# Performance work log

Measured on AMD Instinct MI355X. Metric: run time of the kernel, lower is better.

The kernel has to match this reference:

```python
import jax, jax.numpy as jnp
import numpy as np

N_NODES = 100000
N_EDGES = 3200000
IN_CH = 128
HID = 64
OUT_CH = 2
BN_EPS = 1e-5


def setup_inputs() -> dict:
    key = jax.random.key(0)
    ks = jax.random.split(key, 16)
    def glorot(k, shape):
        fan_in, fan_out = shape[0], shape[1]
        lim = jnp.sqrt(6.0 / (fan_in + fan_out))
        return jax.random.uniform(k, shape, jnp.float32, -lim, lim)
    inp = {
        "x": jax.random.normal(ks[0], (N_NODES, IN_CH), jnp.float32),
        "edge_index": jax.random.randint(ks[1], (2, N_EDGES), 0, N_NODES, jnp.int64),
        # input projection + input BN
        "Wp": glorot(ks[2], (IN_CH, HID)),
        "bp": jnp.zeros((HID,), jnp.float32),
        "g_in": jnp.ones((HID,), jnp.float32),
        "b_in": jnp.zeros((HID,), jnp.float32),
        # SAGEConv layer 0: lin_l (aggr, with bias) + lin_r (self, no bias)
        "Wl0": glorot(ks[3], (HID, HID)),
        "bl0": jnp.zeros((HID,), jnp.float32),
        "Wr0": glorot(ks[4], (HID, HID)),
        "g0": jnp.ones((HID,), jnp.float32),
        "b0": jnp.zeros((HID,), jnp.float32),
        # SAGEConv layer 1
        "Wl1": glorot(ks[5], (HID, HID)),
        "bl1": jnp.zeros((HID,), jnp.float32),
        "Wr1": glorot(ks[6], (HID, HID)),
        "g1": jnp.ones((HID,), jnp.float32),
        "b1": jnp.zeros((HID,), jnp.float32),
        # output head
        "Wo": glorot(ks[7], (HID, OUT_CH)),
        "bo": jnp.zeros((OUT_CH,), jnp.float32),
    }
    return inp


def _bn(h, g, b):
    # training-mode batchnorm over node dim (biased variance, as torch)
    m = h.mean(axis=0)
    v = h.var(axis=0)
    return g * (h - m) * jax.lax.rsqrt(v + BN_EPS) + b


def _sage_conv(h, src, dst, Wl, bl, Wr):
    # mean aggregation of source features at destination nodes
    msg = h[src]                                              # [E, HID]
    summed = jax.ops.segment_sum(msg, dst, num_segments=N_NODES)
    cnt = jax.ops.segment_sum(jnp.ones((src.shape[0],), h.dtype), dst,
                              num_segments=N_NODES)
    aggr = summed / jnp.maximum(cnt, 1.0)[:, None]
    return aggr @ Wl + bl + h @ Wr


def reference(x, edge_index, Wp, bp, g_in, b_in,
              Wl0, bl0, Wr0, g0, b0,
              Wl1, bl1, Wr1, g1, b1,
              Wo, bo):
    src, dst = edge_index[0], edge_index[1]
    h = jax.nn.relu(_bn(x @ Wp + bp, g_in, b_in))   # dropout: eval no-op
    h_prev = h
    # layer 0 (i=0: no residual)
    h_new = jax.nn.relu(_bn(_sage_conv(h, src, dst, Wl0, bl0, Wr0), g0, b0))
    h_prev, h = h, h_new
    # layer 1 (i=1: residual with h_prev)
    h_new = jax.nn.relu(_bn(_sage_conv(h, src, dst, Wl1, bl1, Wr1), g1, b1))
    h_new = h_new + h_prev
    h = h_new
    return h @ Wo + bo
```

## Files before the change

kernel.cpp:

```cpp
#include <hip/hip_runtime.h>
#include <hip/hip_bf16.h>

#define NN 100000
#define NE 3200000
#define IC 128
#define HD 64
#define BN_EPS 1e-5f
#define NBUK 196
#define MSB 16
#define CAP 20480

typedef __attribute__((ext_vector_type(8))) short bf16x8;
typedef __attribute__((ext_vector_type(4))) float f32x4;

#if defined(__has_builtin)
#if __has_builtin(__builtin_amdgcn_fdot2_f32_bf16)
#define HAVE_FDOT2 1
#endif
#endif
#ifndef HAVE_FDOT2
#define HAVE_FDOT2 0
#endif

#if HAVE_FDOT2
typedef __bf16 bf16x2 __attribute__((ext_vector_type(2)));
__device__ __forceinline__ float dot2acc(unsigned int pk, float acc) {
  const unsigned int one2 = 0x3F803F80u;
  return __builtin_amdgcn_fdot2_f32_bf16(__builtin_bit_cast(bf16x2, pk),
                                         __builtin_bit_cast(bf16x2, one2),
                                         acc, false);
}
#endif

__device__ __forceinline__ float bf2f(unsigned short u) {
  return __uint_as_float(((unsigned)u) << 16);
}
__device__ __forceinline__ unsigned int f2bf(float f) {
  unsigned int u = __float_as_uint(f);
  return (u + 0x7FFFu + ((u >> 16) & 1u)) >> 16;
}
__device__ __forceinline__ unsigned int pack2(float a, float b) {
  return f2bf(a) | (f2bf(b) << 16);
}

__global__ __launch_bounds__(512) void k_init(unsigned int* __restrict__ gcur,
                                              float* __restrict__ stats) {
  int t = threadIdx.x;
  if (t < 384) stats[t] = 0.f;
  if (t < NBUK) gcur[t] = (unsigned int)(t * CAP);
}

__global__ __launch_bounds__(256) void k_gemm_in(
    const float* __restrict__ x, const float* __restrict__ Wp,
    const float* __restrict__ bp, unsigned short* __restrict__ pre16,
    float* __restrict__ stats) {
  __shared__ unsigned int sXu[64 * 68];
  __shared__ uint4 sWb[16 * 64];
  __shared__ float sStS[256], sStQ[256];
  int tid = threadIdx.x;
  int wave = tid >> 6, lane = tid & 63;
  int lm = lane & 15, lb = lane >> 4;
  for (int i = tid; i < 1024; i += 256) {
    int b = i >> 6, n = i & 63;
    const float* wp = &Wp[(size_t)(8 * b) * HD + n];
    uint4 p;
    p.x = pack2(wp[0], wp[HD]);
    p.y = pack2(wp[2 * HD], wp[3 * HD]);
    p.z = pack2(wp[4 * HD], wp[5 * HD]);
    p.w = pack2(wp[6 * HD], wp[7 * HD]);
    sWb[i] = p;
  }
  float bias[4];
#pragma unroll
  for (int nt = 0; nt < 4; ++nt) bias[nt] = bp[nt * 16 + lm];
  float S[4] = {0.f, 0.f, 0.f, 0.f}, Q[4] = {0.f, 0.f, 0.f, 0.f};
  const int NT = (NN + 63) / 64;
  for (int t = blockIdx.x; t < NT; t += gridDim.x) {
    int row0 = t * 64;
    __syncthreads();
    for (int i = tid; i < 1024; i += 256) {
      int r = i >> 4, k8 = i & 15;
      int grow = row0 + r;
      uint4 p;
      if (grow < NN) {
        const float* xs = &x[(size_t)grow * IC + k8 * 8];
        float4 f0 = *(const float4*)xs;
        float4 f1 = *(const float4*)(xs + 4);
        p.x = pack2(f0.x, f0.y);
        p.y = pack2(f0.z, f0.w);
        p.z = pack2(f1.x, f1.y);
        p.w = pack2(f1.z, f1.w);
      } else {
        p.x = p.y = p.z = p.w = 0u;
      }
      *(uint4*)&sXu[r * 68 + k8 * 4] = p;
    }
    __syncthreads();
    f32x4 acc[4];
#pragma unroll
    for (int nt = 0; nt < 4; ++nt) acc[nt] = (f32x4){0.f, 0.f, 0.f, 0.f};
#pragma unroll
    for (int ks = 0; ks < 4; ++ks) {
      bf16x8 af =
          *(const bf16x8*)&sXu[(wave * 16 + lm) * 68 + ks * 16 + lb * 4];
      int b = ks * 4 + lb;
#pragma unroll
      for (int nt = 0; nt < 4; ++nt) {
        bf16x8 bf = *(const bf16x8*)&sWb[b * 64 + nt * 16 + lm];
        acc[nt] = __builtin_amdgcn_mfma_f32_16x16x32_bf16(af, bf, acc[nt],
                                                          0, 0, 0);
      }
    }
    int rowl = wave * 16 + lb * 4;
#pragma unroll
    for (int nt = 0; nt < 4; ++nt) {
#pragma unroll
      for (int r = 0; r < 4; ++r) {
        int grow = row0 + rowl + r;
        if (grow < NN) {
          float val = acc[nt][r] + bias[nt];
          pre16[(size_t)grow * HD + nt * 16 + lm] = (unsigned short)f2bf(val);
          S[nt] += val;
          Q[nt] = fmaf(val, val, Q[nt]);
        }
      }
    }
  }
#pragma unroll
  for (int nt = 0; nt < 4; ++nt) {
    S[nt] += __shfl_xor(S[nt], 16);
    S[nt] += __shfl_xor(S[nt], 32);
    Q[nt] += __shfl_xor(Q[nt], 16);
    Q[nt] += __shfl_xor(Q[nt], 32);
  }
  if (lane < 16) {
#pragma unroll
    for (int nt = 0; nt < 4; ++nt) {
      sStS[wave * 64 + nt * 16 + lane] = S[nt];
      sStQ[wave * 64 + nt * 16 + lane] = Q[nt];
    }
  }
  __syncthreads();
  if (tid < 64) {
    float Ts = sStS[tid] + sStS[64 + tid] + sStS[128 + tid] + sStS[192 + tid];
    float Tq = sStQ[tid] + sStQ[64 + tid] + sStQ[128 + tid] + sStQ[192 + tid];
    atomicAdd(&stats[tid], Ts);
    atomicAdd(&stats[64 + tid], Tq);
  }
}

__global__ __launch_bounds__(256) void k_bn_relu(
    const unsigned int* __restrict__ pre16, const float* __restrict__ stats,
    const float* __restrict__ g, const float* __restrict__ b,
    unsigned int* __restrict__ h16u) {
  size_t i = (size_t)blockIdx.x * 256 + threadIdx.x;
  int c0 = ((int)(i & 15)) * 4;
  const float invN = 1.0f / NN;
  uint2 p = *(const uint2*)&pre16[i * 2];
  float v[4];
  v[0] = __uint_as_float(p.x << 16);
  v[1] = __uint_as_float(p.x & 0xFFFF0000u);
  v[2] = __uint_as_float(p.y << 16);
  v[3] = __uint_as_float(p.y & 0xFFFF0000u);
#pragma unroll
  for (int c = 0; c < 4; ++c) {
    float m = stats[c0 + c] * invN;
    float var = stats[64 + c0 + c] * invN - m * m;
    float sc = g[c0 + c] * rsqrtf(var + BN_EPS);
    v[c] = fmaxf((v[c] - m) * sc + b[c0 + c], 0.f);
  }
  uint2 o;
  o.x = pack2(v[0], v[1]);
  o.y = pack2(v[2], v[3]);
  *(uint2*)&h16u[i * 2] = o;
}

__global__ __launch_bounds__(256) void k_msplit(
    const int* __restrict__ src, const int* __restrict__ dst,
    unsigned int* __restrict__ gcur, unsigned int* __restrict__ staging) {
  __shared__ unsigned int hist[NBUK];
  __shared__ unsigned int gbase[NBUK];
  int tid = threadIdx.x;
  for (int i = tid; i < NBUK; i += 256) hist[i] = 0u;
  __syncthreads();
  int e0 = blockIdx.x * (256 * MSB);
  unsigned int pk[MSB], rk[MSB], bk[MSB];
#pragma unroll
  for (int i = 0; i < MSB; ++i) {
    int e = e0 + i * 256 + tid;
    if (e < NE) {
      int d = dst[e];
      unsigned int b = (unsigned int)(d >> 9);
      rk[i] = atomicAdd(&hist[b], 1u);
      pk[i] = (unsigned int)src[e] | ((unsigned int)(d & 511) << 17);
      bk[i] = b;
    } else {
      bk[i] = 0xFFFFFFFFu;
    }
  }
  __syncthreads();
  for (int i = tid; i < NBUK; i += 256)
    if (hist[i]) gbase[i] = atomicAdd(&gcur[i], hist[i]);
  __syncthreads();
#pragma unroll
  for (int i = 0; i < MSB; ++i)
    if (bk[i] != 0xFFFFFFFFu) staging[gbase[bk[i]] + rk[i]] = pk[i];
}

__global__ __launch_bounds__(512) void k_bucket_sort(
    const unsigned int* __restrict__ staging,
    const unsigned int* __restrict__ gcur, unsigned int* __restrict__ nstart,
    unsigned int* __restrict__ srcoff) {
  __shared__ unsigned int hist[512];
  __shared__ unsigned int sc[512];
  __shared__ unsigned int cur[512];
  __shared__ unsigned int bs[256];
  int b = blockIdx.x, t = threadIdx.x;
  hist[t] = 0u;
  if (t < 256)
    bs[t] = (t < NBUK) ? (gcur[t] - (unsigned int)(t * CAP)) : 0u;
  __syncthreads();
  for (int off = 1; off < 256; off <<= 1) {
    unsigned int v = 0u;
    if (t < 256 && t >= off) v = bs[t - off];
    __syncthreads();
    if (t < 256) bs[t] += v;
    __syncthreads();
  }
  int lo = (b == 0) ? 0 : (int)bs[b - 1];
  int cnt = (int)bs[b] - lo;
  int base_in = b * CAP;
  for (int i = t; i < cnt; i += 512)
    atomicAdd(&hist[staging[base_in + i] >> 17], 1u);
  __syncthreads();
  unsigned int my = hist[t];
  sc[t] = my;
  __syncthreads();
  for (int off = 1; off < 512; off <<= 1) {
    unsigned int v = (t >= off) ? sc[t - off] : 0u;
    __syncthreads();
    sc[t] += v;
    __syncthreads();
  }
  unsigned int st = (unsigned int)lo + sc[t] - my;
  cur[t] = st;
  int node = b * 512 + t;
  if (node < NN) {
    nstart[node] = st;
    if (node == NN - 1) nstart[NN] = st + my;
  }
  __syncthreads();
  for (int i = t; i < cnt; i += 512) {
    unsigned int u = staging[base_in + i];
    unsigned int pos = atomicAdd(&cur[u >> 17], 1u);
    srcoff[pos] = (u & 0x1FFFFu) << 7;
  }
}

__global__ __launch_bounds__(256) void k_aggr_sorted(
    const unsigned int* __restrict__ srcoff,
    const unsigned int* __restrict__ nstart,
    const unsigned short* __restrict__ h16,
    unsigned short* __restrict__ a16) {
  int lane = threadIdx.x & 63;
  int n = (int)((blockIdx.x * 256 + threadIdx.x) >> 6);
  if (n >= NN) return;
  int g = lane >> 3;
  int q = lane & 7;
  int e0 = (int)nstart[n];
  int e1 = (int)nstart[n + 1];
  const char* hbase = (const char*)h16 + q * 16;
  float a0 = 0.f, a1 = 0.f, a2 = 0.f, a3 = 0.f;
  float a4 = 0.f, a5 = 0.f, a6 = 0.f, a7 = 0.f;
#if !HAVE_FDOT2
  float b0 = 0.f, b1 = 0.f, b2 = 0.f, b3 = 0.f;
  float b4 = 0.f, b5 = 0.f, b6 = 0.f, b7 = 0.f;
#endif
  int e = e0 + g;
  for (; e + 8 < e1; e += 16) {
    unsigned int o0 = srcoff[e];
    unsigned int o1 = srcoff[e + 8];
    uint4 u0 = *(const uint4*)(hbase + o0);
    uint4 u1 = *(const uint4*)(hbase + o1);
#if HAVE_FDOT2
    a0 = dot2acc(__builtin_amdgcn_perm(u1.x, u0.x, 0x05040100u), a0);
    a1 = dot2acc(__builtin_amdgcn_perm(u1.x, u0.x, 0x07060302u), a1);
    a2 = dot2acc(__builtin_amdgcn_perm(u1.y, u0.y, 0x05040100u), a2);
    a3 = dot2acc(__builtin_amdgcn_perm(u1.y, u0.y, 0x07060302u), a3);
    a4 = dot2acc(__builtin_amdgcn_perm(u1.z, u0.z, 0x05040100u), a4);
    a5 = dot2acc(__builtin_amdgcn_perm(u1.z, u0.z, 0x07060302u), a5);
    a6 = dot2acc(__builtin_amdgcn_perm(u1.w, u0.w, 0x05040100u), a6);
    a7 = dot2acc(__builtin_amdgcn_perm(u1.w, u0.w, 0x07060302u), a7);
#else
    a0 += __uint_as_float(u0.x << 16);
    a1 += __uint_as_float(u0.x & 0xFFFF0000u);
    a2 += __uint_as_float(u0.y << 16);
    a3 += __uint_as_float(u0.y & 0xFFFF0000u);
    a4 += __uint_as_float(u0.z << 16);
    a5 += __uint_as_float(u0.z & 0xFFFF0000u);
    a6 += __uint_as_float(u0.w << 16);
    a7 += __uint_as_float(u0.w & 0xFFFF0000u);
    b0 += __uint_as_float(u1.x << 16);
    b1 += __uint_as_float(u1.x & 0xFFFF0000u);
    b2 += __uint_as_float(u1.y << 16);
    b3 += __uint_as_float(u1.y & 0xFFFF0000u);
    b4 += __uint_as_float(u1.z << 16);
    b5 += __uint_as_float(u1.z & 0xFFFF0000u);
    b6 += __uint_as_float(u1.w << 16);
    b7 += __uint_as_float(u1.w & 0xFFFF0000u);
#endif
  }
  if (e < e1) {
    unsigned int o0 = srcoff[e];
    uint4 u0 = *(const uint4*)(hbase + o0);
#if HAVE_FDOT2
    a0 = dot2acc(__builtin_amdgcn_perm(0u, u0.x, 0x05040100u), a0);
    a1 = dot2acc(__builtin_amdgcn_perm(0u, u0.x, 0x07060302u), a1);
    a2 = dot2acc(__builtin_amdgcn_perm(0u, u0.y, 0x05040100u), a2);
    a3 = dot2acc(__builtin_amdgcn_perm(0u, u0.y, 0x07060302u), a3);
    a4 = dot2acc(__builtin_amdgcn_perm(0u, u0.z, 0x05040100u), a4);
    a5 = dot2acc(__builtin_amdgcn_perm(0u, u0.z, 0x07060302u), a5);
    a6 = dot2acc(__builtin_amdgcn_perm(0u, u0.w, 0x05040100u), a6);
    a7 = dot2acc(__builtin_amdgcn_perm(0u, u0.w, 0x07060302u), a7);
#else
    a0 += __uint_as_float(u0.x << 16);
    a1 += __uint_as_float(u0.x & 0xFFFF0000u);
    a2 += __uint_as_float(u0.y << 16);
    a3 += __uint_as_float(u0.y & 0xFFFF0000u);
    a4 += __uint_as_float(u0.z << 16);
    a5 += __uint_as_float(u0.z & 0xFFFF0000u);
    a6 += __uint_as_float(u0.w << 16);
    a7 += __uint_as_float(u0.w & 0xFFFF0000u);
#endif
  }
#if !HAVE_FDOT2
  a0 += b0; a1 += b1; a2 += b2; a3 += b3;
  a4 += b4; a5 += b5; a6 += b6; a7 += b7;
#endif
#pragma unroll
  for (int off = 8; off <= 32; off <<= 1) {
    a0 += __shfl_xor(a0, off);
    a1 += __shfl_xor(a1, off);
    a2 += __shfl_xor(a2, off);
    a3 += __shfl_xor(a3, off);
    a4 += __shfl_xor(a4, off);
    a5 += __shfl_xor(a5, off);
    a6 += __shfl_xor(a6, off);
    a7 += __shfl_xor(a7, off);
  }
  if (g == 0) {
    float cntf = (float)(e1 - e0);
    float inv = (cntf > 0.f) ? 1.0f / cntf : 0.f;
    uint4 o;
    o.x = pack2(a0 * inv, a1 * inv);
    o.y = pack2(a2 * inv, a3 * inv);
    o.z = pack2(a4 * inv, a5 * inv);
    o.w = pack2(a6 * inv, a7 * inv);
    *(uint4*)((char*)a16 + (size_t)n * 128 + q * 16) = o;
  }
}

__global__ __launch_bounds__(256) void k_combine(
    const unsigned int* __restrict__ a16u,
    const unsigned int* __restrict__ h16u, const float* __restrict__ Wl,
    const float* __restrict__ bl, const float* __restrict__ Wr,
    unsigned short* __restrict__ pre16, float* __restrict__ stats) {
  __shared__ unsigned int sAu[64 * 36], sHu[64 * 36];
  __shared__ uint4 sWb[2 * 8 * 64];
  __shared__ float sStS[256], sStQ[256];
  int tid = threadIdx.x;
  int wave = tid >> 6, lane = tid & 63;
  int lm = lane & 15, lb = lane >> 4;
  for (int i = tid; i < 1024; i += 256) {
    int m = i >> 9, rem = i & 511;
    int b = rem >> 6, n = rem & 63;
    const float* w = (m == 0 ? Wl : Wr) + (size_t)(8 * b) * HD + n;
    uint4 p;
    p.x = pack2(w[0], w[HD]);
    p.y = pack2(w[2 * HD], w[3 * HD]);
    p.z = pack2(w[4 * HD], w[5 * HD]);
    p.w = pack2(w[6 * HD], w[7 * HD]);
    sWb[i] = p;
  }
  float bias[4];
#pragma unroll
  for (int nt = 0; nt < 4; ++nt) bias[nt] = bl[nt * 16 + lm];
  float S[4] = {0.f, 0.f, 0.f, 0.f}, Q[4] = {0.f, 0.f, 0.f, 0.f};
  const int NT = (NN + 63) / 64;
  for (int t = blockIdx.x; t < NT; t += gridDim.x) {
    int row0 = t * 64;
    __syncthreads();
    for (int i = tid; i < 512; i += 256) {
      int r = i >> 3, c4 = i & 7;
      int grow = row0 + r;
      uint4 pa, ph;
      if (grow < NN) {
        pa = *(const uint4*)&a16u[(size_t)grow * 32 + c4 * 4];
        ph = *(const uint4*)&h16u[(size_t)grow * 32 + c4 * 4];
      } else {
        pa.x = pa.y = pa.z = pa.w = 0u;
        ph = pa;
      }
      *(uint4*)&sAu[r * 36 + c4 * 4] = pa;
      *(uint4*)&sHu[r * 36 + c4 * 4] = ph;
    }
    __syncthreads();
    f32x4 acc[4];
#pragma unroll
    for (int nt = 0; nt < 4; ++nt) acc[nt] = (f32x4){0.f, 0.f, 0.f, 0.f};
#pragma unroll
    for (int ks = 0; ks < 2; ++ks) {
      bf16x8 af =
          *(const bf16x8*)&sAu[(wave * 16 + lm) * 36 + ks * 16 + lb * 4];
      bf16x8 hf =
          *(const bf16x8*)&sHu[(wave * 16 + lm) * 36 + ks * 16 + lb * 4];
      int b = ks * 4 + lb;
#pragma unroll
      for (int nt = 0; nt < 4; ++nt) {
        bf16x8 wlf = *(const bf16x8*)&sWb[b * 64 + nt * 16 + lm];
        bf16x8 wrf = *(const bf16x8*)&sWb[512 + b * 64 + nt * 16 + lm];
        acc[nt] = __builtin_amdgcn_mfma_f32_16x16x32_bf16(af, wlf, acc[nt],
                                                          0, 0, 0);
        acc[nt] = __builtin_amdgcn_mfma_f32_16x16x32_bf16(hf, wrf, acc[nt],
                                                          0, 0, 0);
      }
    }
    int rowl = wave * 16 + lb * 4;
#pragma unroll
    for (int nt = 0; nt < 4; ++nt) {
#pragma unroll
      for (int r = 0; r < 4; ++r) {
        int grow = row0 + rowl + r;
        if (grow < NN) {
          float val = acc[nt][r] + bias[nt];
          pre16[(size_t)grow * HD + nt * 16 + lm] = (unsigned short)f2bf(val);
          S[nt] += val;
          Q[nt] = fmaf(val, val, Q[nt]);
        }
      }
    }
  }
#pragma unroll
  for (int nt = 0; nt < 4; ++nt) {
    S[nt] += __shfl_xor(S[nt], 16);
    S[nt] += __shfl_xor(S[nt], 32);
    Q[nt] += __shfl_xor(Q[nt], 16);
    Q[nt] += __shfl_xor(Q[nt], 32);
  }
  if (lane < 16) {
#pragma unroll
    for (int nt = 0; nt < 4; ++nt) {
      sStS[wave * 64 + nt * 16 + lane] = S[nt];
      sStQ[wave * 64 + nt * 16 + lane] = Q[nt];
    }
  }
  __syncthreads();
  if (tid < 64) {
    float Ts = sStS[tid] + sStS[64 + tid] + sStS[128 + tid] + sStS[192 + tid];
    float Tq = sStQ[tid] + sStQ[64 + tid] + sStQ[128 + tid] + sStQ[192 + tid];
    atomicAdd(&stats[tid], Ts);
    atomicAdd(&stats[64 + tid], Tq);
  }
}

__global__ __launch_bounds__(256) void k_bn_relu_head(
    const unsigned short* __restrict__ pre16,
    const float* __restrict__ stats, const float* __restrict__ g,
    const float* __restrict__ b, const unsigned short* __restrict__ resid16,
    const float* __restrict__ Wo, const float* __restrict__ bo,
    float* __restrict__ out) {
  int lane = threadIdx.x & 63;
  int wid = (int)((blockIdx.x * blockDim.x + threadIdx.x) >> 6);
  int nw = (int)((gridDim.x * blockDim.x) >> 6);
  const float invN = 1.0f / NN;
  float m = stats[lane] * invN;
  float v = stats[64 + lane] * invN - m * m;
  float sc = g[lane] * rsqrtf(v + BN_EPS);
  float bb = b[lane];
  float w0 = Wo[lane * 2], w1 = Wo[lane * 2 + 1];
  float b0 = bo[0], b1 = bo[1];
  for (int row = wid; row < NN; row += nw) {
    size_t i = (size_t)row * HD + lane;
    float val = (bf2f(pre16[i]) - m) * sc + bb;
    val = fmaxf(val, 0.f) + bf2f(resid16[i]);
    float a0 = val * w0, a1 = val * w1;
#pragma unroll
    for (int off = 32; off > 0; off >>= 1) {
      a0 += __shfl_down(a0, off);
      a1 += __shfl_down(a1, off);
    }
    if (lane == 0) {
      out[(size_t)row * 2] = a0 + b0;
      out[(size_t)row * 2 + 1] = a1 + b1;
    }
  }
}

extern "C" void kernel_launch(void* const* d_in, const int* in_sizes, int n_in,
                              void* d_out, int out_size, void* d_ws,
                              size_t ws_size, hipStream_t stream) {
  const float* x = (const float*)d_in[0];
  const int* ei = (const int*)d_in[1];
  const float* Wp = (const float*)d_in[2];
  const float* bp = (const float*)d_in[3];
  const float* g_in = (const float*)d_in[4];
  const float* b_in = (const float*)d_in[5];
  const float* Wl0 = (const float*)d_in[6];
  const float* bl0 = (const float*)d_in[7];
  const float* Wr0 = (const float*)d_in[8];
  const float* g0 = (const float*)d_in[9];
  const float* b0 = (const float*)d_in[10];
  const float* Wl1 = (const float*)d_in[11];
  const float* bl1 = (const float*)d_in[12];
  const float* Wr1 = (const float*)d_in[13];
  const float* g1 = (const float*)d_in[14];
  const float* b1 = (const float*)d_in[15];
  const float* Wo = (const float*)d_in[16];
  const float* bo = (const float*)d_in[17];
  float* out = (float*)d_out;

  const int* src = ei;
  const int* dst = ei + NE;

  unsigned int* pre16 = (unsigned int*)d_ws;
  unsigned short* h0 = (unsigned short*)(pre16 + (size_t)NN * 32);
  unsigned short* h1 = h0 + (size_t)NN * HD;
  unsigned short* a16 = h1 + (size_t)NN * HD;
  unsigned int* staging = (unsigned int*)(a16 + (size_t)NN * HD);
  unsigned int* srcoff = staging + (size_t)NBUK * CAP;
  unsigned int* nstart = srcoff + NE;
  unsigned int* gcur = nstart + NN + 1;
  float* stats0 = (float*)(gcur + NBUK);
  float* stats1 = stats0 + 128;
  float* stats2 = stats1 + 128;

  const int BNR_BLOCKS = (NN * HD / 4) / 256;
  const int AGGR_BLOCKS = 25000;
  const int MS_BLOCKS = (NE + 256 * MSB - 1) / (256 * MSB);

  k_init<<<1, 512, 0, stream>>>(gcur, stats0);

  k_gemm_in<<<768, 256, 0, stream>>>(x, Wp, bp, (unsigned short*)pre16,
                                     stats0);
  k_bn_relu<<<BNR_BLOCKS, 256, 0, stream>>>(pre16, stats0, g_in, b_in,
                                            (unsigned int*)h0);

  k_msplit<<<MS_BLOCKS, 256, 0, stream>>>(src, dst, gcur, staging);
  k_bucket_sort<<<NBUK, 512, 0, stream>>>(staging, gcur, nstart, srcoff);

  k_aggr_sorted<<<AGGR_BLOCKS, 256, 0, stream>>>(srcoff, nstart, h0, a16);
  k_combine<<<768, 256, 0, stream>>>((const unsigned int*)a16,
                                     (const unsigned int*)h0, Wl0, bl0, Wr0,
                                     (unsigned short*)pre16, stats1);
  k_bn_relu<<<BNR_BLOCKS, 256, 0, stream>>>(pre16, stats1, g0, b0,
                                            (unsigned int*)h1);

  k_aggr_sorted<<<AGGR_BLOCKS, 256, 0, stream>>>(srcoff, nstart, h1, a16);
  k_combine<<<768, 256, 0, stream>>>((const unsigned int*)a16,
                                     (const unsigned int*)h1, Wl1, bl1, Wr1,
                                     (unsigned short*)pre16, stats2);
  k_bn_relu_head<<<1024, 256, 0, stream>>>((const unsigned short*)pre16,
                                           stats2, g1, b1, h0, Wo, bo, out);
}
```

Baseline: 332.4 us.

## Split hidden features into four column planes and aggregate one plane per pass

Hidden activations are stored as four 16-channel planes (32 bytes per node) instead of 128-byte rows, and the gather-aggregation kernel is launched once over all four planes, each block handling a single plane. The intent is that each plane (about 3.2 MB) stays resident in cache while random source rows are gathered, cutting DRAM traffic from the scattered reads. The cost is that srcoff and nstart are re-read four times, each gather is only 8 bytes, and the BN, combine and head kernels now index through the planar layout.

```diff
diff --git a/kernel.cpp b/kernel.cpp
--- a/kernel.cpp
+++ b/kernel.cpp
@@ -9,6 +9,7 @@
 #define NBUK 196
 #define MSB 16
 #define CAP 20480
+#define NPASS 4
 
 typedef __attribute__((ext_vector_type(8))) short bf16x8;
 typedef __attribute__((ext_vector_type(4))) float f32x4;
@@ -152,9 +153,11 @@
 __global__ __launch_bounds__(256) void k_bn_relu(
     const unsigned int* __restrict__ pre16, const float* __restrict__ stats,
     const float* __restrict__ g, const float* __restrict__ b,
-    unsigned int* __restrict__ h16u) {
+    unsigned int* __restrict__ hpl) {
   size_t i = (size_t)blockIdx.x * 256 + threadIdx.x;
-  int c0 = ((int)(i & 15)) * 4;
+  int chunk = (int)(i & 15);
+  size_t node = i >> 4;
+  int c0 = chunk * 4;
   const float invN = 1.0f / NN;
   uint2 p = *(const uint2*)&pre16[i * 2];
   float v[4];
@@ -172,7 +175,8 @@
   uint2 o;
   o.x = pack2(v[0], v[1]);
   o.y = pack2(v[2], v[3]);
-  *(uint2*)&h16u[i * 2] = o;
+  int plane = chunk >> 2, w = chunk & 3;
+  *(uint2*)&hpl[(size_t)plane * NN * 8 + node * 8 + w * 2] = o;
 }
 
 __global__ __launch_bounds__(256) void k_msplit(
@@ -253,118 +257,96 @@
   for (int i = t; i < cnt; i += 512) {
     unsigned int u = staging[base_in + i];
     unsigned int pos = atomicAdd(&cur[u >> 17], 1u);
-    srcoff[pos] = (u & 0x1FFFFu) << 7;
+    srcoff[pos] = (u & 0x1FFFFu) << 5;
   }
 }
 
 __global__ __launch_bounds__(256) void k_aggr_sorted(
     const unsigned int* __restrict__ srcoff,
     const unsigned int* __restrict__ nstart,
-    const unsigned short* __restrict__ h16,
-    unsigned short* __restrict__ a16) {
-  int lane = threadIdx.x & 63;
-  int n = (int)((blockIdx.x * 256 + threadIdx.x) >> 6);
-  if (n >= NN) return;
-  int g = lane >> 3;
-  int q = lane & 7;
+    const unsigned short* __restrict__ hpl,
+    unsigned short* __restrict__ apl) {
+  int tid = threadIdx.x;
+  int lane = tid & 63;
+  int bid = blockIdx.x;
+  int pass = bid / 25000;
+  int n = (((bid % 25000) * 256 + tid) >> 6);
+  int g = lane >> 2;
+  int q = lane & 3;
   int e0 = (int)nstart[n];
   int e1 = (int)nstart[n + 1];
-  const char* hbase = (const char*)h16 + q * 16;
-  float a0 = 0.f, a1 = 0.f, a2 = 0.f, a3 = 0.f;
-  float a4 = 0.f, a5 = 0.f, a6 = 0.f, a7 = 0.f;
+  const char* hbase =
+      (const char*)(hpl + (size_t)pass * NN * 16) + q * 8;
+  float A0 = 0.f, A1 = 0.f, A2 = 0.f, A3 = 0.f;
 #if !HAVE_FDOT2
-  float b0 = 0.f, b1 = 0.f, b2 = 0.f, b3 = 0.f;
-  float b4 = 0.f, b5 = 0.f, b6 = 0.f, b7 = 0.f;
+  float B0 = 0.f, B1 = 0.f, B2 = 0.f, B3 = 0.f;
 #endif
   int e = e0 + g;
-  for (; e + 8 < e1; e += 16) {
+  for (; e + 16 < e1; e += 32) {
     unsigned int o0 = srcoff[e];
-    unsigned int o1 = srcoff[e + 8];
-    uint4 u0 = *(const uint4*)(hbase + o0);
-    uint4 u1 = *(const uint4*)(hbase + o1);
+    unsigned int o1 = srcoff[e + 16];
+    uint2 u0 = *(const uint2*)(hbase + o0);
+    uint2 u1 = *(const uint2*)(hbase + o1);
 #if HAVE_FDOT2
-    a0 = dot2acc(__builtin_amdgcn_perm(u1.x, u0.x, 0x05040100u), a0);
-    a1 = dot2acc(__builtin_amdgcn_perm(u1.x, u0.x, 0x07060302u), a1);
-    a2 = dot2acc(__builtin_amdgcn_perm(u1.y, u0.y, 0x05040100u), a2);
-    a3 = dot2acc(__builtin_amdgcn_perm(u1.y, u0.y, 0x07060302u), a3);
-    a4 = dot2acc(__builtin_amdgcn_perm(u1.z, u0.z, 0x05040100u), a4);
-    a5 = dot2acc(__builtin_amdgcn_perm(u1.z, u0.z, 0x07060302u), a5);
-    a6 = dot2acc(__builtin_amdgcn_perm(u1.w, u0.w, 0x05040100u), a6);
-    a7 = dot2acc(__builtin_amdgcn_perm(u1.w, u0.w, 0x07060302u), a7);
+    A0 = dot2acc(__builtin_amdgcn_perm(u1.x, u0.x, 0x05040100u), A0);
+    A1 = dot2acc(__builtin_amdgcn_perm(u1.x, u0.x, 0x07060302u), A1);
+    A2 = dot2acc(__builtin_amdgcn_perm(u1.y, u0.y, 0x05040100u), A2);
+    A3 = dot2acc(__builtin_amdgcn_perm(u1.y, u0.y, 0x07060302u), A3);
 #else
-    a0 += __uint_as_float(u0.x << 16);
-    a1 += __uint_as_float(u0.x & 0xFFFF0000u);
-    a2 += __uint_as_float(u0.y << 16);
-    a3 += __uint_as_float(u0.y & 0xFFFF0000u);
-    a4 += __uint_as_float(u0.z << 16);
-    a5 += __uint_as_float(u0.z & 0xFFFF0000u);
-    a6 += __uint_as_float(u0.w << 16);
-    a7 += __uint_as_float(u0.w & 0xFFFF0000u);
-    b0 += __uint_as_float(u1.x << 16);
-    b1 += __uint_as_float(u1.x & 0xFFFF0000u);
-    b2 += __uint_as_float(u1.y << 16);
-    b3 += __uint_as_float(u1.y & 0xFFFF0000u);
-    b4 += __uint_as_float(u1.z << 16);
-    b5 += __uint_as_float(u1.z & 0xFFFF0000u);
-    b6 += __uint_as_float(u1.w << 16);
-    b7 += __uint_as_float(u1.w & 0xFFFF0000u);
+    A0 += __uint_as_float(u0.x << 16);
+    A1 += __uint_as_float(u0.x & 0xFFFF0000u);
+    A2 += __uint_as_float(u0.y << 16);
+    A3 += __uint_as_float(u0.y & 0xFFFF0000u);
+    B0 += __uint_as_float(u1.x << 16);
+    B1 += __uint_as_float(u1.x & 0xFFFF0000u);
+    B2 += __uint_as_float(u1.y << 16);
+    B3 += __uint_as_float(u1.y & 0xFFFF0000u);
 #endif
   }
   if (e < e1) {
     unsigned int o0 = srcoff[e];
-    uint4 u0 = *(const uint4*)(hbase + o0);
+    uint2 u0 = *(const uint2*)(hbase + o0);
 #if HAVE_FDOT2
-    a0 = dot2acc(__builtin_amdgcn_perm(0u, u0.x, 0x05040100u), a0);
-    a1 = dot2acc(__builtin_amdgcn_perm(0u, u0.x, 0x07060302u), a1);
-    a2 = dot2acc(__builtin_amdgcn_perm(0u, u0.y, 0x05040100u), a2);
-    a3 = dot2acc(__builtin_amdgcn_perm(0u, u0.y, 0x07060302u), a3);
-    a4 = dot2acc(__builtin_amdgcn_perm(0u, u0.z, 0x05040100u), a4);
-    a5 = dot2acc(__builtin_amdgcn_perm(0u, u0.z, 0x07060302u), a5);
-    a6 = dot2acc(__builtin_amdgcn_perm(0u, u0.w, 0x05040100u), a6);
-    a7 = dot2acc(__builtin_amdgcn_perm(0u, u0.w, 0x07060302u), a7);
+    A0 = dot2acc(__builtin_amdgcn_perm(0u, u0.x, 0x05040100u), A0);
+    A1 = dot2acc(__builtin_amdgcn_perm(0u, u0.x, 0x07060302u), A1);
+    A2 = dot2acc(__builtin_amdgcn_perm(0u, u0.y, 0x05040100u), A2);
+    A3 = dot2acc(__builtin_amdgcn_perm(0u, u0.y, 0x07060302u), A3);
 #else
-    a0 += __uint_as_float(u0.x << 16);
-    a1 += __uint_as_float(u0.x & 0xFFFF0000u);
-    a2 += __uint_as_float(u0.y << 16);
-    a3 += __uint_as_float(u0.y & 0xFFFF0000u);
-    a4 += __uint_as_float(u0.z << 16);
-    a5 += __uint_as_float(u0.z & 0xFFFF0000u);
-    a6 += __uint_as_float(u0.w << 16);
-    a7 += __uint_as_float(u0.w & 0xFFFF0000u);
+    A0 += __uint_as_float(u0.x << 16);
+    A1 += __uint_as_float(u0.x & 0xFFFF0000u);
+    A2 += __uint_as_float(u0.y << 16);
+    A3 += __uint_as_float(u0.y & 0xFFFF0000u);
 #endif
   }
 #if !HAVE_FDOT2
-  a0 += b0; a1 += b1; a2 += b2; a3 += b3;
-  a4 += b4; a5 += b5; a6 += b6; a7 += b7;
-#endif
-#pragma unroll
-  for (int off = 8; off <= 32; off <<= 1) {
-    a0 += __shfl_xor(a0, off);
-    a1 += __shfl_xor(a1, off);
-    a2 += __shfl_xor(a2, off);
-    a3 += __shfl_xor(a3, off);
-    a4 += __shfl_xor(a4, off);
-    a5 += __shfl_xor(a5, off);
-    a6 += __shfl_xor(a6, off);
-    a7 += __shfl_xor(a7, off);
+  A0 += B0;
+  A1 += B1;
+  A2 += B2;
+  A3 += B3;
+#endif
+#pragma unroll
+  for (int off = 4; off <= 32; off <<= 1) {
+    A0 += __shfl_xor(A0, off);
+    A1 += __shfl_xor(A1, off);
+    A2 += __shfl_xor(A2, off);
+    A3 += __shfl_xor(A3, off);
   }
   if (g == 0) {
     float cntf = (float)(e1 - e0);
     float inv = (cntf > 0.f) ? 1.0f / cntf : 0.f;
-    uint4 o;
-    o.x = pack2(a0 * inv, a1 * inv);
-    o.y = pack2(a2 * inv, a3 * inv);
-    o.z = pack2(a4 * inv, a5 * inv);
-    o.w = pack2(a6 * inv, a7 * inv);
-    *(uint4*)((char*)a16 + (size_t)n * 128 + q * 16) = o;
+    uint2 o;
+    o.x = pack2(A0 * inv, A1 * inv);
+    o.y = pack2(A2 * inv, A3 * inv);
+    *(uint2*)((char*)(apl + (size_t)pass * NN * 16) + (size_t)n * 32 +
+              q * 8) = o;
   }
 }
 
 __global__ __launch_bounds__(256) void k_combine(
-    const unsigned int* __restrict__ a16u,
-    const unsigned int* __restrict__ h16u, const float* __restrict__ Wl,
-    const float* __restrict__ bl, const float* __restrict__ Wr,
-    unsigned short* __restrict__ pre16, float* __restrict__ stats) {
+    const uint4* __restrict__ a4, const uint4* __restrict__ h4,
+    const float* __restrict__ Wl, const float* __restrict__ bl,
+    const float* __restrict__ Wr, unsigned short* __restrict__ pre16,
+    float* __restrict__ stats) {
   __shared__ unsigned int sAu[64 * 36], sHu[64 * 36];
   __shared__ uint4 sWb[2 * 8 * 64];
   __shared__ float sStS[256], sStQ[256];
@@ -393,10 +375,12 @@
     for (int i = tid; i < 512; i += 256) {
       int r = i >> 3, c4 = i & 7;
       int grow = row0 + r;
+      int plane = c4 >> 1, half = c4 & 1;
       uint4 pa, ph;
       if (grow < NN) {
-        pa = *(const uint4*)&a16u[(size_t)grow * 32 + c4 * 4];
-        ph = *(const uint4*)&h16u[(size_t)grow * 32 + c4 * 4];
+        size_t idx = (size_t)plane * NN * 2 + (size_t)grow * 2 + half;
+        pa = a4[idx];
+        ph = h4[idx];
       } else {
         pa.x = pa.y = pa.z = pa.w = 0u;
         ph = pa;
@@ -466,7 +450,7 @@
 __global__ __launch_bounds__(256) void k_bn_relu_head(
     const unsigned short* __restrict__ pre16,
     const float* __restrict__ stats, const float* __restrict__ g,
-    const float* __restrict__ b, const unsigned short* __restrict__ resid16,
+    const float* __restrict__ b, const unsigned short* __restrict__ residpl,
     const float* __restrict__ Wo, const float* __restrict__ bo,
     float* __restrict__ out) {
   int lane = threadIdx.x & 63;
@@ -479,10 +463,12 @@
   float bb = b[lane];
   float w0 = Wo[lane * 2], w1 = Wo[lane * 2 + 1];
   float b0 = bo[0], b1 = bo[1];
+  const unsigned short* rp = residpl + (size_t)(lane >> 4) * NN * 16;
+  int lc = lane & 15;
   for (int row = wid; row < NN; row += nw) {
     size_t i = (size_t)row * HD + lane;
     float val = (bf2f(pre16[i]) - m) * sc + bb;
-    val = fmaxf(val, 0.f) + bf2f(resid16[i]);
+    val = fmaxf(val, 0.f) + bf2f(rp[(size_t)row * 16 + lc]);
     float a0 = val * w0, a1 = val * w1;
 #pragma unroll
     for (int off = 32; off > 0; off >>= 1) {
@@ -535,7 +521,7 @@
   float* stats2 = stats1 + 128;
 
   const int BNR_BLOCKS = (NN * HD / 4) / 256;
-  const int AGGR_BLOCKS = 25000;
+  const int AGGR_BLOCKS = NPASS * 25000;
   const int MS_BLOCKS = (NE + 256 * MSB - 1) / (256 * MSB);
 
   k_init<<<1, 512, 0, stream>>>(gcur, stats0);
@@ -549,16 +535,16 @@
   k_bucket_sort<<<NBUK, 512, 0, stream>>>(staging, gcur, nstart, srcoff);
 
   k_aggr_sorted<<<AGGR_BLOCKS, 256, 0, stream>>>(srcoff, nstart, h0, a16);
-  k_combine<<<768, 256, 0, stream>>>((const unsigned int*)a16,
-                                     (const unsigned int*)h0, Wl0, bl0, Wr0,
-                                     (unsigned short*)pre16, stats1);
+  k_combine<<<768, 256, 0, stream>>>((const uint4*)a16, (const uint4*)h0,
+                                     Wl0, bl0, Wr0, (unsigned short*)pre16,
+                                     stats1);
   k_bn_relu<<<BNR_BLOCKS, 256, 0, stream>>>(pre16, stats1, g0, b0,
                                             (unsigned int*)h1);
 
   k_aggr_sorted<<<AGGR_BLOCKS, 256, 0, stream>>>(srcoff, nstart, h1, a16);
-  k_combine<<<768, 256, 0, stream>>>((const unsigned int*)a16,
-                                     (const unsigned int*)h1, Wl1, bl1, Wr1,
-                                     (unsigned short*)pre16, stats2);
+  k_combine<<<768, 256, 0, stream>>>((const uint4*)a16, (const uint4*)h1,
+                                     Wl1, bl1, Wr1, (unsigned short*)pre16,
+                                     stats2);
   k_bn_relu_head<<<1024, 256, 0, stream>>>((const unsigned short*)pre16,
                                            stats2, g1, b1, h0, Wo, bo, out);
 }
```

Result: slower. 460.3 us (+38.5%).
